# Optimization experiments

Measured on AMD Instinct MI355X. Metric: run time of the kernel, lower is better.

Reference implementation:

```python
import jax, jax.numpy as jnp
import numpy as np

B, L, D, H = 2, 1024, 1024, 16
HD = D // H  # head_dim = 64
EPS = 1e-12  # F.normalize default eps


def setup_inputs() -> dict:
    key = jax.random.key(0)
    ks = jax.random.split(key, 7)
    s = 1.0 / np.sqrt(D)
    return {
        "x": jax.random.normal(ks[0], (B, L, D), dtype=jnp.float32),
        "Wq": jax.random.normal(ks[1], (D, D), dtype=jnp.float32) * s,
        "Wk": jax.random.normal(ks[2], (D, D), dtype=jnp.float32) * s,
        "Wv": jax.random.normal(ks[3], (D, D), dtype=jnp.float32) * s,
        "Wo": jax.random.normal(ks[4], (D, D), dtype=jnp.float32) * s,
        "Wb": jax.random.normal(ks[5], (D, H), dtype=jnp.float32) * s,
        "bb": jnp.zeros((H,), dtype=jnp.float32),
    }


def _l2norm(t):
    # matches F.normalize(t, dim=-1): t / max(||t||_2, eps)
    n = jnp.sqrt(jnp.sum(t * t, axis=-1, keepdims=True))
    return t / jnp.maximum(n, EPS)


def reference(x, Wq, Wk, Wv, Wo, Wb, bb):
    q = (x @ Wq).reshape(B, L, H, HD)
    k = (x @ Wk).reshape(B, L, H, HD)
    v = (x @ Wv).reshape(B, L, H, HD)
    beta = jax.nn.sigmoid(x @ Wb + bb)          # [B, L, H]
    q = _l2norm(q)
    k = _l2norm(k)
    # gated outer products: [B, L, H, HD, HD]
    kv = jnp.einsum('blhd,blhe->blhde', k, v) * beta[..., None, None]
    kv_cumsum = jnp.cumsum(kv, axis=1)          # causal cumulative kv state
    out = jnp.einsum('blhd,blhde->blhe', q, kv_cumsum)  # [B, L, H, HD]
    return out.reshape(B, L, D) @ Wo
```

## Files before the change

kernel.cpp:

```cpp
#include <hip/hip_runtime.h>
#include <math.h>

#define BB   2
#define LL   1024
#define DD   1024
#define HH   16
#define HDIM 64
#define MM   (BB * LL)
#define CHK  64
#define NCHK (LL / CHK)

typedef short bf16x8 __attribute__((ext_vector_type(8)));
typedef float f32x4  __attribute__((ext_vector_type(4)));
typedef const __attribute__((address_space(1))) unsigned int* gas_ptr;
typedef __attribute__((address_space(3))) unsigned int* las_ptr;

__device__ __forceinline__ void gload16(const void* g, void* l) {
    __builtin_amdgcn_global_load_lds((gas_ptr)(unsigned long long)g,
                                     (las_ptr)(unsigned long long)l, 16, 0, 0);
}

__device__ __forceinline__ unsigned short f2bf(float f) {
    unsigned int u = __float_as_uint(f);
    u += 0x7fffu + ((u >> 16) & 1u);
    return (unsigned short)(u >> 16);
}
__device__ __forceinline__ float bfhi(unsigned int u) { return __uint_as_float(u & 0xffff0000u); }
__device__ __forceinline__ float bflo(unsigned int u) { return __uint_as_float(u << 16); }

__device__ __forceinline__ bf16x8 frag70(const unsigned short* a, int row, int tc) {
    const unsigned int* p = (const unsigned int*)(a + row * 70 + tc);
    union { unsigned int u[4]; bf16x8 v; } r;
    r.u[0] = p[0]; r.u[1] = p[1]; r.u[2] = p[2]; r.u[3] = p[3];
    return r.v;
}

__global__ void prep_kernel(const float* __restrict__ x, unsigned short* __restrict__ xb,
                            const float* __restrict__ Wb, float* __restrict__ Wbt) {
    const int bid = blockIdx.x;
    if (bid < 2048) {
        const int idx = bid * 256 + threadIdx.x;
        const float4 v = ((const float4*)x)[idx];
        ushort4 o;
        o.x = f2bf(v.x); o.y = f2bf(v.y); o.z = f2bf(v.z); o.w = f2bf(v.w);
        ((ushort4*)xb)[idx] = o;
    } else {
        const int t = (bid - 2048) * 256 + threadIdx.x;
        const int h = t >> 10, k = t & 1023;
        Wbt[t] = Wb[k * HH + h];
    }
}

__global__ void transpose_cast(const float* __restrict__ W0, const float* __restrict__ W1,
                               const float* __restrict__ W2, const float* __restrict__ W3,
                               unsigned short* __restrict__ T0, unsigned short* __restrict__ T1,
                               unsigned short* __restrict__ T2, unsigned short* __restrict__ T3) {
    __shared__ float tile[32][33];
    const int which = blockIdx.x >> 10;
    const int b = blockIdx.x & 1023;
    const int bk = b >> 5, bn = b & 31;
    const float* W = which == 0 ? W0 : which == 1 ? W1 : which == 2 ? W2 : W3;
    unsigned short* T = which == 0 ? T0 : which == 1 ? T1 : which == 2 ? T2 : T3;
    const int tx = threadIdx.x & 31, ty = threadIdx.x >> 5;
#pragma unroll
    for (int i = 0; i < 4; ++i)
        tile[ty + i * 8][tx] = W[(size_t)(bk * 32 + ty + i * 8) * DD + bn * 32 + tx];
    __syncthreads();
#pragma unroll
    for (int i = 0; i < 4; ++i)
        T[(size_t)(bn * 32 + ty + i * 8) * DD + bk * 32 + tx] = f2bf(tile[tx][ty + i * 8]);
}

__device__ __forceinline__ void gemm_kloop(const unsigned short* A, const unsigned short* Bt,
                                           unsigned short* As, unsigned short* Bs,
                                           int rowBase, int colBase, int K,
                                           f32x4 acc[4][4]) {
    const int tid = threadIdx.x;
    const int c0 = tid, c1 = tid + 256;
    const int ar0 = c0 >> 2, ak0 = (c0 & 3) << 3;
    const int ar1 = c1 >> 2, ak1 = (c1 & 3) << 3;
    const unsigned short* Ag0 = A + (size_t)(rowBase + ar0) * K + ak0;
    const unsigned short* Ag1 = A + (size_t)(rowBase + ar1) * K + ak1;
    const unsigned short* Bg0 = Bt + (size_t)(colBase + ar0) * K + ak0;
    const unsigned short* Bg1 = Bt + (size_t)(colBase + ar1) * K + ak1;
    unsigned short* Al0 = As + c0 * 8; unsigned short* Al1 = As + c1 * 8;
    unsigned short* Bl0 = Bs + c0 * 8; unsigned short* Bl1 = Bs + c1 * 8;
    const int lane = tid & 63, wv = tid >> 6;
    const int qr = wv >> 1, qc = wv & 1;
    const int fr = lane & 15;
    const int koff = (lane >> 4) << 3;
    int aoff[4], boff[4];
#pragma unroll
    for (int mi = 0; mi < 4; ++mi) aoff[mi] = (qr * 64 + mi * 16 + fr) * 32 + koff;
#pragma unroll
    for (int nj = 0; nj < 4; ++nj) boff[nj] = (qc * 64 + nj * 16 + fr) * 32 + koff;

    for (int k0 = 0; k0 < K; k0 += 32) {
        __syncthreads();
        gload16(Ag0, Al0); gload16(Ag1, Al1);
        gload16(Bg0, Bl0); gload16(Bg1, Bl1);
        Ag0 += 32; Ag1 += 32; Bg0 += 32; Bg1 += 32;
        __syncthreads();
        bf16x8 av[4], bv[4];
#pragma unroll
        for (int mi = 0; mi < 4; ++mi) av[mi] = *(const bf16x8*)(As + aoff[mi]);
#pragma unroll
        for (int nj = 0; nj < 4; ++nj) bv[nj] = *(const bf16x8*)(Bs + boff[nj]);
#pragma unroll
        for (int mi = 0; mi < 4; ++mi)
#pragma unroll
            for (int nj = 0; nj < 4; ++nj)
                acc[mi][nj] = __builtin_amdgcn_mfma_f32_16x16x32_bf16(av[mi], bv[nj], acc[mi][nj], 0, 0, 0);
    }
}

__global__ __launch_bounds__(256) void gemm_qkv(const unsigned short* __restrict__ xb,
                                                const unsigned short* __restrict__ Wqt,
                                                const unsigned short* __restrict__ Wkt,
                                                const unsigned short* __restrict__ Wvt,
                                                unsigned short* __restrict__ qb,
                                                unsigned short* __restrict__ kb,
                                                unsigned short* __restrict__ vb) {
    __shared__ unsigned short As[128 * 32];
    __shared__ unsigned short Bs[128 * 32];
    const int by = blockIdx.x / 24, bxx = blockIdx.x % 24;
    const int mat = bxx >> 3, tn = bxx & 7;
    const unsigned short* Bt = mat == 0 ? Wqt : (mat == 1 ? Wkt : Wvt);
    unsigned short* Cout = mat == 0 ? qb : (mat == 1 ? kb : vb);
    f32x4 acc[4][4];
#pragma unroll
    for (int mi = 0; mi < 4; ++mi)
#pragma unroll
        for (int nj = 0; nj < 4; ++nj) acc[mi][nj] = (f32x4){0.f, 0.f, 0.f, 0.f};
    gemm_kloop(xb, Bt, As, Bs, by * 128, tn * 128, DD, acc);

    const int lane = threadIdx.x & 63, wv = threadIdx.x >> 6;
    const int qr = wv >> 1, qc = wv & 1;
    if (mat < 2) {
#pragma unroll
        for (int mi = 0; mi < 4; ++mi)
#pragma unroll
            for (int i = 0; i < 4; ++i) {
                float s = 0.f;
#pragma unroll
                for (int nj = 0; nj < 4; ++nj) { float t = acc[mi][nj][i]; s += t * t; }
                s += __shfl_xor(s, 1, 64);
                s += __shfl_xor(s, 2, 64);
                s += __shfl_xor(s, 4, 64);
                s += __shfl_xor(s, 8, 64);
                const float inv = 1.0f / fmaxf(sqrtf(s), 1e-12f);
#pragma unroll
                for (int nj = 0; nj < 4; ++nj) acc[mi][nj][i] *= inv;
            }
    }
#pragma unroll
    for (int mi = 0; mi < 4; ++mi)
#pragma unroll
        for (int i = 0; i < 4; ++i) {
            const int row = by * 128 + qr * 64 + mi * 16 + (lane >> 4) * 4 + i;
#pragma unroll
            for (int nj = 0; nj < 4; ++nj) {
                const int col = tn * 128 + qc * 64 + nj * 16 + (lane & 15);
                Cout[(size_t)row * DD + col] = f2bf(acc[mi][nj][i]);
            }
        }
}

__global__ __launch_bounds__(256) void gemm_out(const unsigned short* __restrict__ yb,
                                                const unsigned short* __restrict__ Wot,
                                                float* __restrict__ out) {
    __shared__ unsigned short As[64 * 32];
    __shared__ unsigned short Bs[128 * 32];
    const int by = blockIdx.x >> 3, tn = blockIdx.x & 7;
    const int tid = threadIdx.x;
    const int rowBase = by * 64, colBase = tn * 128;
    const int ar = tid >> 2, ak = (tid & 3) << 3;
    const unsigned short* Ag = yb + (size_t)(rowBase + ar) * DD + ak;
    unsigned short* Al = As + tid * 8;
    const int c1 = tid + 256;
    const int br1 = c1 >> 2, bk1 = (c1 & 3) << 3;
    const unsigned short* Bg0 = Wot + (size_t)(colBase + ar) * DD + ak;
    const unsigned short* Bg1 = Wot + (size_t)(colBase + br1) * DD + bk1;
    unsigned short* Bl0 = Bs + tid * 8; unsigned short* Bl1 = Bs + c1 * 8;
    const int lane = tid & 63, wv = tid >> 6;
    const int rh = wv & 1, ch = wv >> 1;
    const int fr = lane & 15, koff = (lane >> 4) << 3;
    int aoff[2], boff[4];
#pragma unroll
    for (int mi = 0; mi < 2; ++mi) aoff[mi] = (rh * 32 + mi * 16 + fr) * 32 + koff;
#pragma unroll
    for (int nj = 0; nj < 4; ++nj) boff[nj] = (ch * 64 + nj * 16 + fr) * 32 + koff;
    f32x4 acc[2][4];
#pragma unroll
    for (int mi = 0; mi < 2; ++mi)
#pragma unroll
        for (int nj = 0; nj < 4; ++nj) acc[mi][nj] = (f32x4){0.f, 0.f, 0.f, 0.f};
    for (int k0 = 0; k0 < DD; k0 += 32) {
        __syncthreads();
        gload16(Ag, Al); gload16(Bg0, Bl0); gload16(Bg1, Bl1);
        Ag += 32; Bg0 += 32; Bg1 += 32;
        __syncthreads();
        bf16x8 av[2], bv[4];
#pragma unroll
        for (int mi = 0; mi < 2; ++mi) av[mi] = *(const bf16x8*)(As + aoff[mi]);
#pragma unroll
        for (int nj = 0; nj < 4; ++nj) bv[nj] = *(const bf16x8*)(Bs + boff[nj]);
#pragma unroll
        for (int mi = 0; mi < 2; ++mi)
#pragma unroll
            for (int nj = 0; nj < 4; ++nj)
                acc[mi][nj] = __builtin_amdgcn_mfma_f32_16x16x32_bf16(av[mi], bv[nj], acc[mi][nj], 0, 0, 0);
    }
    const int quad = lane >> 4;
#pragma unroll
    for (int mi = 0; mi < 2; ++mi)
#pragma unroll
        for (int i = 0; i < 4; ++i) {
            const int row = rowBase + rh * 32 + mi * 16 + quad * 4 + i;
#pragma unroll
            for (int nj = 0; nj < 4; ++nj) {
                const int col = colBase + ch * 64 + nj * 16 + fr;
                out[(size_t)row * DD + col] = acc[mi][nj][i];
            }
        }
}

__global__ void beta_kernel(const float* __restrict__ x, const float* __restrict__ Wbt,
                            const float* __restrict__ bias, float* __restrict__ beta) {
    const int m = blockIdx.x * 4 + (threadIdx.x >> 6);
    const int lane = threadIdx.x & 63;
    const float4* xr = (const float4*)(x + (size_t)m * DD);
    float4 xv[4];
#pragma unroll
    for (int i = 0; i < 4; ++i) xv[i] = xr[lane * 4 + i];
    float res = 0.f;
#pragma unroll
    for (int h = 0; h < HH; ++h) {
        const float4* wr = (const float4*)(Wbt + (size_t)h * DD);
        float s = 0.f;
#pragma unroll
        for (int i = 0; i < 4; ++i) {
            const float4 w = wr[lane * 4 + i];
            s += xv[i].x * w.x + xv[i].y * w.y + xv[i].z * w.z + xv[i].w * w.w;
        }
        s += __shfl_xor(s, 1, 64);  s += __shfl_xor(s, 2, 64);
        s += __shfl_xor(s, 4, 64);  s += __shfl_xor(s, 8, 64);
        s += __shfl_xor(s, 16, 64); s += __shfl_xor(s, 32, 64);
        if (lane == h) res = s;
    }
    if (lane < HH) beta[m * HH + lane] = 1.0f / (1.0f + expf(-(res + bias[lane])));
}

__global__ __launch_bounds__(256) void chunkkv_kernel(const unsigned short* __restrict__ k,
                                                      const unsigned short* __restrict__ v,
                                                      const float* __restrict__ beta,
                                                      float* __restrict__ states) {
    const int c = blockIdx.x % NCHK;
    const int bh = blockIdx.x / NCHK;
    const int b = bh / HH, h = bh % HH;
    __shared__ unsigned short kT[64 * 70];
    __shared__ unsigned short vT[64 * 70];
    const int tid = threadIdx.x;
    for (int i = tid; i < 512; i += 256) {
        const int t = i >> 3, dg = (i & 7) << 3;
        const int m = b * LL + c * CHK + t;
        const float be = beta[m * HH + h];
        const size_t go = (size_t)m * DD + h * 64 + dg;
        const uint4 ku = *(const uint4*)&k[go];
        const uint4 vu = *(const uint4*)&v[go];
        unsigned int kw[4] = {ku.x, ku.y, ku.z, ku.w};
        unsigned int vw[4] = {vu.x, vu.y, vu.z, vu.w};
#pragma unroll
        for (int jj = 0; jj < 4; ++jj) {
            kT[(dg + 2 * jj)     * 70 + t] = f2bf(bflo(kw[jj]) * be);
            kT[(dg + 2 * jj + 1) * 70 + t] = f2bf(bfhi(kw[jj]) * be);
            vT[(dg + 2 * jj)     * 70 + t] = (unsigned short)(vw[jj] & 0xffffu);
            vT[(dg + 2 * jj + 1) * 70 + t] = (unsigned short)(vw[jj] >> 16);
        }
    }
    __syncthreads();
    const int lane = tid & 63, wv = tid >> 6;
    const int fr = lane & 15, quad = lane >> 4;
    f32x4 acc[4];
#pragma unroll
    for (int et = 0; et < 4; ++et) acc[et] = (f32x4){0.f, 0.f, 0.f, 0.f};
#pragma unroll
    for (int kh = 0; kh < 2; ++kh) {
        const int tc = kh * 32 + quad * 8;
        const bf16x8 a = frag70(kT, wv * 16 + fr, tc);
#pragma unroll
        for (int et = 0; et < 4; ++et) {
            const bf16x8 bb = frag70(vT, et * 16 + fr, tc);
            acc[et] = __builtin_amdgcn_mfma_f32_16x16x32_bf16(a, bb, acc[et], 0, 0, 0);
        }
    }
    float* outp = states + ((size_t)bh * NCHK + c) * 4096;
#pragma unroll
    for (int et = 0; et < 4; ++et)
#pragma unroll
        for (int i = 0; i < 4; ++i) {
            const int d = wv * 16 + quad * 4 + i;
            const int e = et * 16 + fr;
            outp[d * 64 + e] = acc[et][i];
        }
}

__global__ void prefix_kernel(float* __restrict__ states) {
    const int bh = blockIdx.x >> 4, pg = blockIdx.x & 15;
    float* base = states + (size_t)bh * NCHK * 4096 + pg * 256 + threadIdx.x;
    float vals[NCHK];
#pragma unroll
    for (int c = 0; c < NCHK; ++c) vals[c] = base[c * 4096];
    float run = 0.0f;
#pragma unroll
    for (int c = 0; c < NCHK; ++c) {
        base[c * 4096] = run;
        run += vals[c];
    }
}

__global__ __launch_bounds__(256) void attn_kernel(const unsigned short* __restrict__ q,
                                                   const unsigned short* __restrict__ k,
                                                   const unsigned short* __restrict__ v,
                                                   const float* __restrict__ beta,
                                                   const float* __restrict__ states,
                                                   unsigned short* __restrict__ y) {
    const int c = blockIdx.x % NCHK;
    const int bh = blockIdx.x / NCHK;
    const int b = bh / HH, h = bh % HH;
    __shared__ unsigned short qS[64 * 80];
    __shared__ unsigned short kS[64 * 80];
    __shared__ unsigned short sS[64 * 80];
    __shared__ unsigned short vT[64 * 70];
    __shared__ unsigned short sT[64 * 70];
    const int tid = threadIdx.x;
    const float* stg = states + ((size_t)bh * NCHK + c) * 4096;
    for (int i = tid; i < 512; i += 256) {
        const int t = i >> 3, dg = (i & 7) << 3;
        const int m = b * LL + c * CHK + t;
        const float be = beta[m * HH + h];
        const size_t go = (size_t)m * DD + h * 64 + dg;
        const uint4 qu = *(const uint4*)&q[go];
        const uint4 ku = *(const uint4*)&k[go];
        const uint4 vu = *(const uint4*)&v[go];
        *(uint4*)&qS[t * 80 + dg] = qu;
        *(uint4*)&kS[t * 80 + dg] = ku;
        unsigned int vw[4] = {vu.x, vu.y, vu.z, vu.w};
#pragma unroll
        for (int jj = 0; jj < 4; ++jj) {
            vT[(dg + 2 * jj)     * 70 + t] = f2bf(bflo(vw[jj]) * be);
            vT[(dg + 2 * jj + 1) * 70 + t] = f2bf(bfhi(vw[jj]) * be);
        }
    }
    for (int i = tid; i < 1024; i += 256) {
        const int d = i >> 4, eg = (i & 15) << 2;
        const float4 s4 = ((const float4*)stg)[i];
        sT[(eg + 0) * 70 + d] = f2bf(s4.x);
        sT[(eg + 1) * 70 + d] = f2bf(s4.y);
        sT[(eg + 2) * 70 + d] = f2bf(s4.z);
        sT[(eg + 3) * 70 + d] = f2bf(s4.w);
    }
    __syncthreads();
    const int lane = tid & 63, wv = tid >> 6;
    const int fr = lane & 15, quad = lane >> 4;
    const int koff = quad * 8;
    f32x4 s_acc[4];
#pragma unroll
    for (int j = 0; j < 4; ++j) s_acc[j] = (f32x4){0.f, 0.f, 0.f, 0.f};
#pragma unroll
    for (int kh = 0; kh < 2; ++kh) {
        const bf16x8 a = *(const bf16x8*)&qS[(wv * 16 + fr) * 80 + kh * 32 + koff];
#pragma unroll
        for (int j = 0; j < 4; ++j) {
            const bf16x8 bb = *(const bf16x8*)&kS[(j * 16 + fr) * 80 + kh * 32 + koff];
            s_acc[j] = __builtin_amdgcn_mfma_f32_16x16x32_bf16(a, bb, s_acc[j], 0, 0, 0);
        }
    }
#pragma unroll
    for (int j = 0; j < 4; ++j)
#pragma unroll
        for (int i = 0; i < 4; ++i) {
            const int t = wv * 16 + quad * 4 + i;
            const int s = j * 16 + fr;
            sS[t * 80 + s] = (s <= t) ? f2bf(s_acc[j][i]) : (unsigned short)0;
        }
    f32x4 o_acc[4];
#pragma unroll
    for (int j = 0; j < 4; ++j) o_acc[j] = (f32x4){0.f, 0.f, 0.f, 0.f};
#pragma unroll
    for (int kh = 0; kh < 2; ++kh) {
        const bf16x8 a = *(const bf16x8*)&sS[(wv * 16 + fr) * 80 + kh * 32 + koff];
#pragma unroll
        for (int j = 0; j < 4; ++j) {
            const bf16x8 bb = frag70(vT, j * 16 + fr, kh * 32 + koff);
            o_acc[j] = __builtin_amdgcn_mfma_f32_16x16x32_bf16(a, bb, o_acc[j], 0, 0, 0);
        }
    }
#pragma unroll
    for (int kh = 0; kh < 2; ++kh) {
        const bf16x8 a = *(const bf16x8*)&qS[(wv * 16 + fr) * 80 + kh * 32 + koff];
#pragma unroll
        for (int j = 0; j < 4; ++j) {
            const bf16x8 bb = frag70(sT, j * 16 + fr, kh * 32 + koff);
            o_acc[j] = __builtin_amdgcn_mfma_f32_16x16x32_bf16(a, bb, o_acc[j], 0, 0, 0);
        }
    }
#pragma unroll
    for (int j = 0; j < 4; ++j)
#pragma unroll
        for (int i = 0; i < 4; ++i) {
            const int m = b * LL + c * CHK + wv * 16 + quad * 4 + i;
            const int e = j * 16 + fr;
            y[(size_t)m * DD + h * 64 + e] = f2bf(o_acc[j][i]);
        }
}

extern "C" void kernel_launch(void* const* d_in, const int* in_sizes, int n_in,
                              void* d_out, int out_size, void* d_ws, size_t ws_size,
                              hipStream_t stream) {
    (void)in_sizes; (void)n_in; (void)out_size; (void)ws_size;
    const float* x  = (const float*)d_in[0];
    const float* Wq = (const float*)d_in[1];
    const float* Wk = (const float*)d_in[2];
    const float* Wv = (const float*)d_in[3];
    const float* Wo = (const float*)d_in[4];
    const float* Wb = (const float*)d_in[5];
    const float* bbp = (const float*)d_in[6];
    float* out = (float*)d_out;

    char* ws = (char*)d_ws;
    unsigned short* xb  = (unsigned short*)ws;                      ws += (size_t)MM * DD * 2;
    unsigned short* Wqt = (unsigned short*)ws;                      ws += (size_t)DD * DD * 2;
    unsigned short* Wkt = (unsigned short*)ws;                      ws += (size_t)DD * DD * 2;
    unsigned short* Wvt = (unsigned short*)ws;                      ws += (size_t)DD * DD * 2;
    unsigned short* Wot = (unsigned short*)ws;                      ws += (size_t)DD * DD * 2;
    float*          Wbt = (float*)ws;                               ws += (size_t)HH * DD * 4;
    unsigned short* qb  = (unsigned short*)ws;                      ws += (size_t)MM * DD * 2;
    unsigned short* kb  = (unsigned short*)ws;                      ws += (size_t)MM * DD * 2;
    unsigned short* vb  = (unsigned short*)ws;                      ws += (size_t)MM * DD * 2;
    unsigned short* yb  = (unsigned short*)ws;                      ws += (size_t)MM * DD * 2;
    float*          beta   = (float*)ws;                            ws += (size_t)MM * HH * 4;
    float*          states = (float*)ws;                            ws += (size_t)BB * HH * NCHK * 4096 * 4;

    prep_kernel<<<2112, 256, 0, stream>>>(x, xb, Wb, Wbt);
    transpose_cast<<<4096, 256, 0, stream>>>(Wq, Wk, Wv, Wo, Wqt, Wkt, Wvt, Wot);
    gemm_qkv<<<16 * 24, 256, 0, stream>>>(xb, Wqt, Wkt, Wvt, qb, kb, vb);
    beta_kernel<<<MM / 4, 256, 0, stream>>>(x, Wbt, bbp, beta);
    chunkkv_kernel<<<BB * HH * NCHK, 256, 0, stream>>>(kb, vb, beta, states);
    prefix_kernel<<<BB * HH * NCHK, 256, 0, stream>>>(states);
    attn_kernel<<<BB * HH * NCHK, 256, 0, stream>>>(qb, kb, vb, beta, states, yb);
    gemm_out<<<32 * 8, 256, 0, stream>>>(yb, Wot, out);
}
```

Before: 155.3 us.

## Merge prep kernels, fold beta GEMM into QKV launch, drop prefix kernel

Combines the x cast, Wb transpose and weight transpose-cast into one launch, and computes beta with MFMA on bf16 x and Wb in 16 extra blocks of the QKV GEMM launch. The separate fp32 beta kernel goes away. The prefix-scan kernel is removed: each attention block now sums the preceding chunk states itself, in registers. This cuts three launches and the scan's extra write/read pass. In exchange, late chunks read up to 15 states each (quadratic state traffic), and beta now uses bf16 inputs, which costs some precision.

```diff
diff --git a/kernel.cpp b/kernel.cpp
--- a/kernel.cpp
+++ b/kernel.cpp
@@ -35,8 +35,12 @@
     return r.v;
 }
 
-__global__ void prep_kernel(const float* __restrict__ x, unsigned short* __restrict__ xb,
-                            const float* __restrict__ Wb, float* __restrict__ Wbt) {
+__global__ void prep_all(const float* __restrict__ x, unsigned short* __restrict__ xb,
+                         const float* __restrict__ Wb, unsigned short* __restrict__ Wbt,
+                         const float* __restrict__ W0, const float* __restrict__ W1,
+                         const float* __restrict__ W2, const float* __restrict__ W3,
+                         unsigned short* __restrict__ T0, unsigned short* __restrict__ T1,
+                         unsigned short* __restrict__ T2, unsigned short* __restrict__ T3) {
     const int bid = blockIdx.x;
     if (bid < 2048) {
         const int idx = bid * 256 + threadIdx.x;
@@ -44,20 +48,18 @@
         ushort4 o;
         o.x = f2bf(v.x); o.y = f2bf(v.y); o.z = f2bf(v.z); o.w = f2bf(v.w);
         ((ushort4*)xb)[idx] = o;
-    } else {
+        return;
+    }
+    if (bid < 2112) {
         const int t = (bid - 2048) * 256 + threadIdx.x;
-        const int h = t >> 10, k = t & 1023;
-        Wbt[t] = Wb[k * HH + h];
-    }
-}
-
-__global__ void transpose_cast(const float* __restrict__ W0, const float* __restrict__ W1,
-                               const float* __restrict__ W2, const float* __restrict__ W3,
-                               unsigned short* __restrict__ T0, unsigned short* __restrict__ T1,
-                               unsigned short* __restrict__ T2, unsigned short* __restrict__ T3) {
+        const int h = t >> 10, kidx = t & 1023;
+        Wbt[t] = f2bf(Wb[kidx * HH + h]);
+        return;
+    }
     __shared__ float tile[32][33];
-    const int which = blockIdx.x >> 10;
-    const int b = blockIdx.x & 1023;
+    const int b4 = bid - 2112;
+    const int which = b4 >> 10;
+    const int b = b4 & 1023;
     const int bk = b >> 5, bn = b & 31;
     const float* W = which == 0 ? W0 : which == 1 ? W1 : which == 2 ? W2 : W3;
     unsigned short* T = which == 0 ? T0 : which == 1 ? T1 : which == 2 ? T2 : T3;
@@ -114,15 +116,45 @@
     }
 }
 
-__global__ __launch_bounds__(256) void gemm_qkv(const unsigned short* __restrict__ xb,
-                                                const unsigned short* __restrict__ Wqt,
-                                                const unsigned short* __restrict__ Wkt,
-                                                const unsigned short* __restrict__ Wvt,
-                                                unsigned short* __restrict__ qb,
-                                                unsigned short* __restrict__ kb,
-                                                unsigned short* __restrict__ vb) {
+__global__ __launch_bounds__(256) void gemm_qkv_beta(const unsigned short* __restrict__ xb,
+                                                     const unsigned short* __restrict__ Wqt,
+                                                     const unsigned short* __restrict__ Wkt,
+                                                     const unsigned short* __restrict__ Wvt,
+                                                     const unsigned short* __restrict__ Wbt,
+                                                     const float* __restrict__ bbp,
+                                                     unsigned short* __restrict__ qb,
+                                                     unsigned short* __restrict__ kb,
+                                                     unsigned short* __restrict__ vb,
+                                                     float* __restrict__ beta) {
     __shared__ unsigned short As[128 * 32];
     __shared__ unsigned short Bs[128 * 32];
+    const int lane = threadIdx.x & 63, wv = threadIdx.x >> 6;
+    const int fr = lane & 15, quad = lane >> 4;
+    if (blockIdx.x >= 384) {
+        const int rowBase = (blockIdx.x - 384) * 128;
+        const int r0 = rowBase + wv * 32 + fr;
+        f32x4 bacc[2];
+        bacc[0] = (f32x4){0.f, 0.f, 0.f, 0.f};
+        bacc[1] = (f32x4){0.f, 0.f, 0.f, 0.f};
+        for (int k0 = 0; k0 < DD; k0 += 32) {
+            const int kk = k0 + quad * 8;
+            const bf16x8 a0 = *(const bf16x8*)&xb[(size_t)r0 * DD + kk];
+            const bf16x8 a1 = *(const bf16x8*)&xb[(size_t)(r0 + 16) * DD + kk];
+            const bf16x8 bw = *(const bf16x8*)&Wbt[(size_t)fr * DD + kk];
+            bacc[0] = __builtin_amdgcn_mfma_f32_16x16x32_bf16(a0, bw, bacc[0], 0, 0, 0);
+            bacc[1] = __builtin_amdgcn_mfma_f32_16x16x32_bf16(a1, bw, bacc[1], 0, 0, 0);
+        }
+        const float bias = bbp[fr];
+#pragma unroll
+        for (int mi = 0; mi < 2; ++mi)
+#pragma unroll
+            for (int i = 0; i < 4; ++i) {
+                const int row = rowBase + wv * 32 + mi * 16 + quad * 4 + i;
+                const float s = bacc[mi][i] + bias;
+                beta[row * HH + fr] = 1.0f / (1.0f + expf(-s));
+            }
+        return;
+    }
     const int by = blockIdx.x / 24, bxx = blockIdx.x % 24;
     const int mat = bxx >> 3, tn = bxx & 7;
     const unsigned short* Bt = mat == 0 ? Wqt : (mat == 1 ? Wkt : Wvt);
@@ -134,7 +166,6 @@
         for (int nj = 0; nj < 4; ++nj) acc[mi][nj] = (f32x4){0.f, 0.f, 0.f, 0.f};
     gemm_kloop(xb, Bt, As, Bs, by * 128, tn * 128, DD, acc);
 
-    const int lane = threadIdx.x & 63, wv = threadIdx.x >> 6;
     const int qr = wv >> 1, qc = wv & 1;
     if (mat < 2) {
 #pragma unroll
@@ -157,12 +188,169 @@
     for (int mi = 0; mi < 4; ++mi)
 #pragma unroll
         for (int i = 0; i < 4; ++i) {
-            const int row = by * 128 + qr * 64 + mi * 16 + (lane >> 4) * 4 + i;
+            const int row = by * 128 + qr * 64 + mi * 16 + quad * 4 + i;
 #pragma unroll
             for (int nj = 0; nj < 4; ++nj) {
-                const int col = tn * 128 + qc * 64 + nj * 16 + (lane & 15);
+                const int col = tn * 128 + qc * 64 + nj * 16 + fr;
                 Cout[(size_t)row * DD + col] = f2bf(acc[mi][nj][i]);
             }
+        }
+}
+
+__global__ __launch_bounds__(256) void chunkkv_kernel(const unsigned short* __restrict__ k,
+                                                      const unsigned short* __restrict__ v,
+                                                      const float* __restrict__ beta,
+                                                      float* __restrict__ states) {
+    const int c = blockIdx.x % NCHK;
+    const int bh = blockIdx.x / NCHK;
+    const int b = bh / HH, h = bh % HH;
+    __shared__ unsigned short kT[64 * 70];
+    __shared__ unsigned short vT[64 * 70];
+    const int tid = threadIdx.x;
+    for (int i = tid; i < 512; i += 256) {
+        const int t = i >> 3, dg = (i & 7) << 3;
+        const int m = b * LL + c * CHK + t;
+        const float be = beta[m * HH + h];
+        const size_t go = (size_t)m * DD + h * 64 + dg;
+        const uint4 ku = *(const uint4*)&k[go];
+        const uint4 vu = *(const uint4*)&v[go];
+        unsigned int kw[4] = {ku.x, ku.y, ku.z, ku.w};
+        unsigned int vw[4] = {vu.x, vu.y, vu.z, vu.w};
+#pragma unroll
+        for (int jj = 0; jj < 4; ++jj) {
+            kT[(dg + 2 * jj)     * 70 + t] = f2bf(bflo(kw[jj]) * be);
+            kT[(dg + 2 * jj + 1) * 70 + t] = f2bf(bfhi(kw[jj]) * be);
+            vT[(dg + 2 * jj)     * 70 + t] = (unsigned short)(vw[jj] & 0xffffu);
+            vT[(dg + 2 * jj + 1) * 70 + t] = (unsigned short)(vw[jj] >> 16);
+        }
+    }
+    __syncthreads();
+    const int lane = tid & 63, wv = tid >> 6;
+    const int fr = lane & 15, quad = lane >> 4;
+    f32x4 acc[4];
+#pragma unroll
+    for (int et = 0; et < 4; ++et) acc[et] = (f32x4){0.f, 0.f, 0.f, 0.f};
+#pragma unroll
+    for (int kh = 0; kh < 2; ++kh) {
+        const int tc = kh * 32 + quad * 8;
+        const bf16x8 a = frag70(kT, wv * 16 + fr, tc);
+#pragma unroll
+        for (int et = 0; et < 4; ++et) {
+            const bf16x8 bb = frag70(vT, et * 16 + fr, tc);
+            acc[et] = __builtin_amdgcn_mfma_f32_16x16x32_bf16(a, bb, acc[et], 0, 0, 0);
+        }
+    }
+    float* outp = states + ((size_t)bh * NCHK + c) * 4096;
+#pragma unroll
+    for (int et = 0; et < 4; ++et)
+#pragma unroll
+        for (int i = 0; i < 4; ++i) {
+            const int d = wv * 16 + quad * 4 + i;
+            const int e = et * 16 + fr;
+            outp[d * 64 + e] = acc[et][i];
+        }
+}
+
+__global__ __launch_bounds__(256) void attn_kernel(const unsigned short* __restrict__ q,
+                                                   const unsigned short* __restrict__ k,
+                                                   const unsigned short* __restrict__ v,
+                                                   const float* __restrict__ beta,
+                                                   const float* __restrict__ states,
+                                                   unsigned short* __restrict__ y) {
+    const int c = blockIdx.x % NCHK;
+    const int bh = blockIdx.x / NCHK;
+    const int b = bh / HH, h = bh % HH;
+    __shared__ unsigned short qS[64 * 80];
+    __shared__ unsigned short kS[64 * 80];
+    __shared__ unsigned short sS[64 * 80];
+    __shared__ unsigned short vT[64 * 70];
+    __shared__ unsigned short sT[64 * 70];
+    const int tid = threadIdx.x;
+    for (int i = tid; i < 512; i += 256) {
+        const int t = i >> 3, dg = (i & 7) << 3;
+        const int m = b * LL + c * CHK + t;
+        const float be = beta[m * HH + h];
+        const size_t go = (size_t)m * DD + h * 64 + dg;
+        const uint4 qu = *(const uint4*)&q[go];
+        const uint4 ku = *(const uint4*)&k[go];
+        const uint4 vu = *(const uint4*)&v[go];
+        *(uint4*)&qS[t * 80 + dg] = qu;
+        *(uint4*)&kS[t * 80 + dg] = ku;
+        unsigned int vw[4] = {vu.x, vu.y, vu.z, vu.w};
+#pragma unroll
+        for (int jj = 0; jj < 4; ++jj) {
+            vT[(dg + 2 * jj)     * 70 + t] = f2bf(bflo(vw[jj]) * be);
+            vT[(dg + 2 * jj + 1) * 70 + t] = f2bf(bfhi(vw[jj]) * be);
+        }
+    }
+    {
+        float racc[16];
+#pragma unroll
+        for (int j = 0; j < 16; ++j) racc[j] = 0.f;
+        const float* sbase = states + (size_t)bh * NCHK * 4096;
+        for (int cc = 0; cc < c; ++cc) {
+            const float* sp = sbase + cc * 4096;
+#pragma unroll
+            for (int j = 0; j < 16; ++j) racc[j] += sp[j * 256 + tid];
+        }
+        const int e = tid & 63;
+        const int dbase = tid >> 6;
+#pragma unroll
+        for (int j = 0; j < 16; ++j)
+            sT[e * 70 + j * 4 + dbase] = f2bf(racc[j]);
+    }
+    __syncthreads();
+    const int lane = tid & 63, wv = tid >> 6;
+    const int fr = lane & 15, quad = lane >> 4;
+    const int koff = quad * 8;
+    f32x4 s_acc[4];
+#pragma unroll
+    for (int j = 0; j < 4; ++j) s_acc[j] = (f32x4){0.f, 0.f, 0.f, 0.f};
+#pragma unroll
+    for (int kh = 0; kh < 2; ++kh) {
+        const bf16x8 a = *(const bf16x8*)&qS[(wv * 16 + fr) * 80 + kh * 32 + koff];
+#pragma unroll
+        for (int j = 0; j < 4; ++j) {
+            const bf16x8 bb = *(const bf16x8*)&kS[(j * 16 + fr) * 80 + kh * 32 + koff];
+            s_acc[j] = __builtin_amdgcn_mfma_f32_16x16x32_bf16(a, bb, s_acc[j], 0, 0, 0);
+        }
+    }
+#pragma unroll
+    for (int j = 0; j < 4; ++j)
+#pragma unroll
+        for (int i = 0; i < 4; ++i) {
+            const int t = wv * 16 + quad * 4 + i;
+            const int s = j * 16 + fr;
+            sS[t * 80 + s] = (s <= t) ? f2bf(s_acc[j][i]) : (unsigned short)0;
+        }
+    f32x4 o_acc[4];
+#pragma unroll
+    for (int j = 0; j < 4; ++j) o_acc[j] = (f32x4){0.f, 0.f, 0.f, 0.f};
+#pragma unroll
+    for (int kh = 0; kh < 2; ++kh) {
+        const bf16x8 a = *(const bf16x8*)&sS[(wv * 16 + fr) * 80 + kh * 32 + koff];
+#pragma unroll
+        for (int j = 0; j < 4; ++j) {
+            const bf16x8 bb = frag70(vT, j * 16 + fr, kh * 32 + koff);
+            o_acc[j] = __builtin_amdgcn_mfma_f32_16x16x32_bf16(a, bb, o_acc[j], 0, 0, 0);
+        }
+    }
+#pragma unroll
+    for (int kh = 0; kh < 2; ++kh) {
+        const bf16x8 a = *(const bf16x8*)&qS[(wv * 16 + fr) * 80 + kh * 32 + koff];
+#pragma unroll
+        for (int j = 0; j < 4; ++j) {
+            const bf16x8 bb = frag70(sT, j * 16 + fr, kh * 32 + koff);
+            o_acc[j] = __builtin_amdgcn_mfma_f32_16x16x32_bf16(a, bb, o_acc[j], 0, 0, 0);
+        }
+    }
+#pragma unroll
+    for (int j = 0; j < 4; ++j)
+#pragma unroll
+        for (int i = 0; i < 4; ++i) {
+            const int m = b * LL + c * CHK + wv * 16 + quad * 4 + i;
+            const int e = j * 16 + fr;
+            y[(size_t)m * DD + h * 64 + e] = f2bf(o_acc[j][i]);
         }
 }
 
@@ -225,196 +413,6 @@
         }
 }
 
-__global__ void beta_kernel(const float* __restrict__ x, const float* __restrict__ Wbt,
-                            const float* __restrict__ bias, float* __restrict__ beta) {
-    const int m = blockIdx.x * 4 + (threadIdx.x >> 6);
-    const int lane = threadIdx.x & 63;
-    const float4* xr = (const float4*)(x + (size_t)m * DD);
-    float4 xv[4];
-#pragma unroll
-    for (int i = 0; i < 4; ++i) xv[i] = xr[lane * 4 + i];
-    float res = 0.f;
-#pragma unroll
-    for (int h = 0; h < HH; ++h) {
-        const float4* wr = (const float4*)(Wbt + (size_t)h * DD);
-        float s = 0.f;
-#pragma unroll
-        for (int i = 0; i < 4; ++i) {
-            const float4 w = wr[lane * 4 + i];
-            s += xv[i].x * w.x + xv[i].y * w.y + xv[i].z * w.z + xv[i].w * w.w;
-        }
-        s += __shfl_xor(s, 1, 64);  s += __shfl_xor(s, 2, 64);
-        s += __shfl_xor(s, 4, 64);  s += __shfl_xor(s, 8, 64);
-        s += __shfl_xor(s, 16, 64); s += __shfl_xor(s, 32, 64);
-        if (lane == h) res = s;
-    }
-    if (lane < HH) beta[m * HH + lane] = 1.0f / (1.0f + expf(-(res + bias[lane])));
-}
-
-__global__ __launch_bounds__(256) void chunkkv_kernel(const unsigned short* __restrict__ k,
-                                                      const unsigned short* __restrict__ v,
-                                                      const float* __restrict__ beta,
-                                                      float* __restrict__ states) {
-    const int c = blockIdx.x % NCHK;
-    const int bh = blockIdx.x / NCHK;
-    const int b = bh / HH, h = bh % HH;
-    __shared__ unsigned short kT[64 * 70];
-    __shared__ unsigned short vT[64 * 70];
-    const int tid = threadIdx.x;
-    for (int i = tid; i < 512; i += 256) {
-        const int t = i >> 3, dg = (i & 7) << 3;
-        const int m = b * LL + c * CHK + t;
-        const float be = beta[m * HH + h];
-        const size_t go = (size_t)m * DD + h * 64 + dg;
-        const uint4 ku = *(const uint4*)&k[go];
-        const uint4 vu = *(const uint4*)&v[go];
-        unsigned int kw[4] = {ku.x, ku.y, ku.z, ku.w};
-        unsigned int vw[4] = {vu.x, vu.y, vu.z, vu.w};
-#pragma unroll
-        for (int jj = 0; jj < 4; ++jj) {
-            kT[(dg + 2 * jj)     * 70 + t] = f2bf(bflo(kw[jj]) * be);
-            kT[(dg + 2 * jj + 1) * 70 + t] = f2bf(bfhi(kw[jj]) * be);
-            vT[(dg + 2 * jj)     * 70 + t] = (unsigned short)(vw[jj] & 0xffffu);
-            vT[(dg + 2 * jj + 1) * 70 + t] = (unsigned short)(vw[jj] >> 16);
-        }
-    }
-    __syncthreads();
-    const int lane = tid & 63, wv = tid >> 6;
-    const int fr = lane & 15, quad = lane >> 4;
-    f32x4 acc[4];
-#pragma unroll
-    for (int et = 0; et < 4; ++et) acc[et] = (f32x4){0.f, 0.f, 0.f, 0.f};
-#pragma unroll
-    for (int kh = 0; kh < 2; ++kh) {
-        const int tc = kh * 32 + quad * 8;
-        const bf16x8 a = frag70(kT, wv * 16 + fr, tc);
-#pragma unroll
-        for (int et = 0; et < 4; ++et) {
-            const bf16x8 bb = frag70(vT, et * 16 + fr, tc);
-            acc[et] = __builtin_amdgcn_mfma_f32_16x16x32_bf16(a, bb, acc[et], 0, 0, 0);
-        }
-    }
-    float* outp = states + ((size_t)bh * NCHK + c) * 4096;
-#pragma unroll
-    for (int et = 0; et < 4; ++et)
-#pragma unroll
-        for (int i = 0; i < 4; ++i) {
-            const int d = wv * 16 + quad * 4 + i;
-            const int e = et * 16 + fr;
-            outp[d * 64 + e] = acc[et][i];
-        }
-}
-
-__global__ void prefix_kernel(float* __restrict__ states) {
-    const int bh = blockIdx.x >> 4, pg = blockIdx.x & 15;
-    float* base = states + (size_t)bh * NCHK * 4096 + pg * 256 + threadIdx.x;
-    float vals[NCHK];
-#pragma unroll
-    for (int c = 0; c < NCHK; ++c) vals[c] = base[c * 4096];
-    float run = 0.0f;
-#pragma unroll
-    for (int c = 0; c < NCHK; ++c) {
-        base[c * 4096] = run;
-        run += vals[c];
-    }
-}
-
-__global__ __launch_bounds__(256) void attn_kernel(const unsigned short* __restrict__ q,
-                                                   const unsigned short* __restrict__ k,
-                                                   const unsigned short* __restrict__ v,
-                                                   const float* __restrict__ beta,
-                                                   const float* __restrict__ states,
-                                                   unsigned short* __restrict__ y) {
-    const int c = blockIdx.x % NCHK;
-    const int bh = blockIdx.x / NCHK;
-    const int b = bh / HH, h = bh % HH;
-    __shared__ unsigned short qS[64 * 80];
-    __shared__ unsigned short kS[64 * 80];
-    __shared__ unsigned short sS[64 * 80];
-    __shared__ unsigned short vT[64 * 70];
-    __shared__ unsigned short sT[64 * 70];
-    const int tid = threadIdx.x;
-    const float* stg = states + ((size_t)bh * NCHK + c) * 4096;
-    for (int i = tid; i < 512; i += 256) {
-        const int t = i >> 3, dg = (i & 7) << 3;
-        const int m = b * LL + c * CHK + t;
-        const float be = beta[m * HH + h];
-        const size_t go = (size_t)m * DD + h * 64 + dg;
-        const uint4 qu = *(const uint4*)&q[go];
-        const uint4 ku = *(const uint4*)&k[go];
-        const uint4 vu = *(const uint4*)&v[go];
-        *(uint4*)&qS[t * 80 + dg] = qu;
-        *(uint4*)&kS[t * 80 + dg] = ku;
-        unsigned int vw[4] = {vu.x, vu.y, vu.z, vu.w};
-#pragma unroll
-        for (int jj = 0; jj < 4; ++jj) {
-            vT[(dg + 2 * jj)     * 70 + t] = f2bf(bflo(vw[jj]) * be);
-            vT[(dg + 2 * jj + 1) * 70 + t] = f2bf(bfhi(vw[jj]) * be);
-        }
-    }
-    for (int i = tid; i < 1024; i += 256) {
-        const int d = i >> 4, eg = (i & 15) << 2;
-        const float4 s4 = ((const float4*)stg)[i];
-        sT[(eg + 0) * 70 + d] = f2bf(s4.x);
-        sT[(eg + 1) * 70 + d] = f2bf(s4.y);
-        sT[(eg + 2) * 70 + d] = f2bf(s4.z);
-        sT[(eg + 3) * 70 + d] = f2bf(s4.w);
-    }
-    __syncthreads();
-    const int lane = tid & 63, wv = tid >> 6;
-    const int fr = lane & 15, quad = lane >> 4;
-    const int koff = quad * 8;
-    f32x4 s_acc[4];
-#pragma unroll
-    for (int j = 0; j < 4; ++j) s_acc[j] = (f32x4){0.f, 0.f, 0.f, 0.f};
-#pragma unroll
-    for (int kh = 0; kh < 2; ++kh) {
-        const bf16x8 a = *(const bf16x8*)&qS[(wv * 16 + fr) * 80 + kh * 32 + koff];
-#pragma unroll
-        for (int j = 0; j < 4; ++j) {
-            const bf16x8 bb = *(const bf16x8*)&kS[(j * 16 + fr) * 80 + kh * 32 + koff];
-            s_acc[j] = __builtin_amdgcn_mfma_f32_16x16x32_bf16(a, bb, s_acc[j], 0, 0, 0);
-        }
-    }
-#pragma unroll
-    for (int j = 0; j < 4; ++j)
-#pragma unroll
-        for (int i = 0; i < 4; ++i) {
-            const int t = wv * 16 + quad * 4 + i;
-            const int s = j * 16 + fr;
-            sS[t * 80 + s] = (s <= t) ? f2bf(s_acc[j][i]) : (unsigned short)0;
-        }
-    f32x4 o_acc[4];
-#pragma unroll
-    for (int j = 0; j < 4; ++j) o_acc[j] = (f32x4){0.f, 0.f, 0.f, 0.f};
-#pragma unroll
-    for (int kh = 0; kh < 2; ++kh) {
-        const bf16x8 a = *(const bf16x8*)&sS[(wv * 16 + fr) * 80 + kh * 32 + koff];
-#pragma unroll
-        for (int j = 0; j < 4; ++j) {
-            const bf16x8 bb = frag70(vT, j * 16 + fr, kh * 32 + koff);
-            o_acc[j] = __builtin_amdgcn_mfma_f32_16x16x32_bf16(a, bb, o_acc[j], 0, 0, 0);
-        }
-    }
-#pragma unroll
-    for (int kh = 0; kh < 2; ++kh) {
-        const bf16x8 a = *(const bf16x8*)&qS[(wv * 16 + fr) * 80 + kh * 32 + koff];
-#pragma unroll
-        for (int j = 0; j < 4; ++j) {
-            const bf16x8 bb = frag70(sT, j * 16 + fr, kh * 32 + koff);
-            o_acc[j] = __builtin_amdgcn_mfma_f32_16x16x32_bf16(a, bb, o_acc[j], 0, 0, 0);
-        }
-    }
-#pragma unroll
-    for (int j = 0; j < 4; ++j)
-#pragma unroll
-        for (int i = 0; i < 4; ++i) {
-            const int m = b * LL + c * CHK + wv * 16 + quad * 4 + i;
-            const int e = j * 16 + fr;
-            y[(size_t)m * DD + h * 64 + e] = f2bf(o_acc[j][i]);
-        }
-}
-
 extern "C" void kernel_launch(void* const* d_in, const int* in_sizes, int n_in,
                               void* d_out, int out_size, void* d_ws, size_t ws_size,
                               hipStream_t stream) {
@@ -434,7 +432,7 @@
     unsigned short* Wkt = (unsigned short*)ws;                      ws += (size_t)DD * DD * 2;
     unsigned short* Wvt = (unsigned short*)ws;                      ws += (size_t)DD * DD * 2;
     unsigned short* Wot = (unsigned short*)ws;                      ws += (size_t)DD * DD * 2;
-    float*          Wbt = (float*)ws;                               ws += (size_t)HH * DD * 4;
+    unsigned short* Wbt = (unsigned short*)ws;                      ws += (size_t)HH * DD * 2;
     unsigned short* qb  = (unsigned short*)ws;                      ws += (size_t)MM * DD * 2;
     unsigned short* kb  = (unsigned short*)ws;                      ws += (size_t)MM * DD * 2;
     unsigned short* vb  = (unsigned short*)ws;                      ws += (size_t)MM * DD * 2;
@@ -442,12 +440,9 @@
     float*          beta   = (float*)ws;                            ws += (size_t)MM * HH * 4;
     float*          states = (float*)ws;                            ws += (size_t)BB * HH * NCHK * 4096 * 4;
 
-    prep_kernel<<<2112, 256, 0, stream>>>(x, xb, Wb, Wbt);
-    transpose_cast<<<4096, 256, 0, stream>>>(Wq, Wk, Wv, Wo, Wqt, Wkt, Wvt, Wot);
-    gemm_qkv<<<16 * 24, 256, 0, stream>>>(xb, Wqt, Wkt, Wvt, qb, kb, vb);
-    beta_kernel<<<MM / 4, 256, 0, stream>>>(x, Wbt, bbp, beta);
+    prep_all<<<6208, 256, 0, stream>>>(x, xb, Wb, Wbt, Wq, Wk, Wv, Wo, Wqt, Wkt, Wvt, Wot);
+    gemm_qkv_beta<<<400, 256, 0, stream>>>(xb, Wqt, Wkt, Wvt, Wbt, bbp, qb, kb, vb, beta);
     chunkkv_kernel<<<BB * HH * NCHK, 256, 0, stream>>>(kb, vb, beta, states);
-    prefix_kernel<<<BB * HH * NCHK, 256, 0, stream>>>(states);
     attn_kernel<<<BB * HH * NCHK, 256, 0, stream>>>(qb, kb, vb, beta, states, yb);
     gemm_out<<<32 * 8, 256, 0, stream>>>(yb, Wot, out);
 }
```

Result: faster. 145.9 us (-6.1%).
